# Kernel tuning notes

Hardware: AMD Instinct MI355X
Metric: run time of the kernel (lower is better)

The kernel has to match this reference:

```python
import jax, jax.numpy as jnp
import numpy as np

K = 16

def _pairwise_sqdist(a, b):
    # a:[B,n,3] b:[B,m,3] -> [B,n,m]
    return (jnp.sum(a * a, -1)[:, :, None] + jnp.sum(b * b, -1)[:, None, :]
            - 2.0 * jnp.einsum('bnd,bmd->bnm', a, b))

def _group(x, idx):
    # x:[B,N,C], idx:[B,M,K] -> [B,M,K,C]
    return jax.vmap(lambda xb, ib: xb[ib])(x, idx)

def _gather(x, idx):
    # x:[B,N,C], idx:[B,M] -> [B,M,C]
    return jax.vmap(lambda xb, ib: xb[ib])(x, idx)

def _knn_idx(pos, k):
    p = jax.lax.stop_gradient(pos)
    d = _pairwise_sqdist(p, p)
    return jax.lax.top_k(-d, k)[1]

def _leaky(v):
    return jnp.where(v >= 0, v, 0.2 * v)

def _edge_conv(x, pos, w_self, w_edge, idx=None):
    if idx is None:
        idx = _knn_idx(pos, K)
    nx = _group(x, idx)                      # [B,N,K,C]
    npos = _group(pos, idx)                  # [B,N,K,3]
    rel = pos[:, :, None, :] - npos
    d2 = jnp.sum(rel * rel, -1, keepdims=True)
    h = jnp.concatenate([nx, rel, d2], -1)   # [B,N,K,C+4]
    term_n = jnp.mean(h @ w_edge, axis=2)
    return _leaky(x @ w_self + term_n)

def _fps(pos, npoint):
    # furthest point sampling, starts at index 0 (matches pointnet2 CUDA op)
    pos = jax.lax.stop_gradient(pos)
    B, N, _ = pos.shape
    def body(carry, _):
        dists, far = carry
        c = jnp.take_along_axis(pos, far[:, None, None], axis=1)  # [B,1,3]
        d = jnp.sum((pos - c) ** 2, -1)
        dists = jnp.minimum(dists, d)
        return (dists, jnp.argmax(dists, axis=1).astype(jnp.int32)), far
    init = (jnp.full((B, N), 1e10, pos.dtype), jnp.zeros((B,), jnp.int32))
    _, idxs = jax.lax.scan(body, init, None, length=npoint)
    return jnp.transpose(idxs)  # [B,npoint]

def _three_nn(unknown, known):
    d = _pairwise_sqdist(unknown, known)
    negd, idx = jax.lax.top_k(-d, 3)
    dist = jnp.maximum(-negd, 0.0)  # squared dists, as in pointnet2 kernel
    return jax.lax.stop_gradient(dist), idx  # three_nn is non-differentiable

def _interp_weights(dist):
    recip = 1.0 / (dist + 1e-8)
    return recip / jnp.sum(recip, axis=2, keepdims=True)

def _three_interp(feat, idx, weight):
    g = _group(feat, idx)  # [B,n,3,C]
    return jnp.sum(weight[..., None] * g, axis=2)

def _forward(x, pos, w_self0, w_edge0, w_self1, w_edge1, w_self2, w_edge2,
             w_up1, b_up1, w_upc1_self, w_upc1_edge,
             w_up0, b_up0, w_upc0_self, w_upc0_edge, w_out, b_out):
    feat0 = _edge_conv(x, pos, w_self0, w_edge0)
    pos0 = pos
    n1 = pos0.shape[1] // 2
    idx1 = _fps(pos0, n1)
    pos1 = _gather(pos0, idx1)
    feat1 = _edge_conv(_gather(feat0, idx1), pos1, w_self1, w_edge1)
    n2 = pos1.shape[1] // 2
    idx2 = _fps(pos1, n2)
    pos2 = _gather(pos1, idx2)
    feat2 = _edge_conv(_gather(feat1, idx2), pos2, w_self2, w_edge2)
    dist, idx = _three_nn(pos1, pos2)
    w = _interp_weights(dist)
    cat1 = jnp.concatenate([_three_interp(feat2, idx, w), feat1], -1)
    feat_up1 = _leaky(cat1 @ w_up1 + b_up1)
    feat_up1 = _edge_conv(feat_up1, pos1, w_upc1_self, w_upc1_edge)
    dist, idx = _three_nn(pos0, pos1)
    w = _interp_weights(dist)
    cat0 = jnp.concatenate([_three_interp(feat_up1, idx, w), feat0], -1)
    feat_up0 = _leaky(cat0 @ w_up0 + b_up0)
    feat_out = _edge_conv(feat_up0, pos0, w_upc0_self, w_upc0_edge)
    return feat_out @ w_out + b_out

def setup_inputs() -> dict:
    B, N, CIN, D = 2, 8192, 4, 64
    key = jax.random.key(0)
    ks = jax.random.split(key, 20)
    def w(k, fin, fout):
        return jax.random.normal(k, (fin, fout), jnp.float32) / np.sqrt(fin)
    return {
        'x': jax.random.normal(ks[0], (B, N, CIN), jnp.float32),
        'pos': jax.random.normal(ks[1], (B, N, 3), jnp.float32),
        'w_self0': w(ks[2], CIN, D),        'w_edge0': w(ks[3], CIN + 4, D),
        'w_self1': w(ks[4], D, 2 * D),      'w_edge1': w(ks[5], D + 4, 2 * D),
        'w_self2': w(ks[6], 2 * D, 4 * D),  'w_edge2': w(ks[7], 2 * D + 4, 4 * D),
        'w_up1': w(ks[8], 6 * D, 2 * D),    'b_up1': jnp.zeros((2 * D,), jnp.float32),
        'w_upc1_self': w(ks[9], 2 * D, 2 * D), 'w_upc1_edge': w(ks[10], 2 * D + 4, 2 * D),
        'w_up0': w(ks[11], 3 * D, D),       'b_up0': jnp.zeros((D,), jnp.float32),
        'w_upc0_self': w(ks[12], D, D),     'w_upc0_edge': w(ks[13], D + 4, D),
        'w_out': w(ks[14], D, 128),         'b_out': jnp.zeros((128,), jnp.float32),
    }

def reference(x, pos, w_self0, w_edge0, w_self1, w_edge1, w_self2, w_edge2,
              w_up1, b_up1, w_upc1_self, w_upc1_edge,
              w_up0, b_up0, w_upc0_self, w_upc0_edge, w_out, b_out):
    return _forward(x, pos, w_self0, w_edge0, w_self1, w_edge1, w_self2, w_edge2,
                    w_up1, b_up1, w_upc1_self, w_upc1_edge,
                    w_up0, b_up0, w_upc0_self, w_upc0_edge, w_out, b_out)
```

## Files before the change

### kernel.cpp

```cpp
#include <hip/hip_runtime.h>
#include <cstdint>

typedef unsigned long long u64;

static __device__ __forceinline__ float leakyf(float v) { return v >= 0.f ? v : 0.2f * v; }

__global__ void pack_kernel(const float* __restrict__ pos, int total, float4* __restrict__ out)
{
  int i = blockIdx.x * 256 + threadIdx.x;
  if (i >= total) return;
  float x = pos[i*3+0], y = pos[i*3+1], z = pos[i*3+2];
  out[i] = make_float4(x, y, z, (x*x + y*y) + z*z);
}

template<int CTRL>
static __device__ __forceinline__ u64 dpp_max_u64_step(u64 x)
{
  unsigned lo = (unsigned)x, hi = (unsigned)(x >> 32);
  unsigned ylo = (unsigned)__builtin_amdgcn_update_dpp((int)lo, (int)lo, CTRL, 0xF, 0xF, false);
  unsigned yhi = (unsigned)__builtin_amdgcn_update_dpp((int)hi, (int)hi, CTRL, 0xF, 0xF, false);
  u64 y = ((u64)yhi << 32) | (u64)ylo;
  return x > y ? x : y;
}
static __device__ __forceinline__ u64 wave64_max_u64(u64 x)
{
  x = dpp_max_u64_step<0x111>(x);
  x = dpp_max_u64_step<0x112>(x);
  x = dpp_max_u64_step<0x114>(x);
  x = dpp_max_u64_step<0x118>(x);
  x = dpp_max_u64_step<0x142>(x);
  x = dpp_max_u64_step<0x143>(x);
  unsigned lo = (unsigned)__builtin_amdgcn_readlane((int)(unsigned)x, 63);
  unsigned hi = (unsigned)__builtin_amdgcn_readlane((int)(unsigned)(x >> 32), 63);
  return ((u64)hi << 32) | (u64)lo;
}

template<int N, int NPOINT>
__global__ __launch_bounds__(256) void fps_kernel(const float* __restrict__ pos,
                                                  int* __restrict__ out_idx,
                                                  float* __restrict__ out_pos,
                                                  float4* __restrict__ out_pp)
{
  constexpr int BLOCK = 256;
  constexpr int NPT = N / BLOCK;
  const int b = blockIdx.x;
  const float* P = pos + (size_t)b * N * 3;
  int* oi = out_idx + (size_t)b * NPOINT;
  float* op = out_pos + (size_t)b * NPOINT * 3;
  float4* opp = out_pp + (size_t)b * NPOINT;

  __shared__ float4 spos[N];
  __shared__ __align__(16) u64 redk[2][4];

  const int t = threadIdx.x;
  const int lane = t & 63;
  const int wv = t >> 6;

  float px[NPT], py[NPT], pz[NPT], dist[NPT];
  unsigned iv[NPT];
#pragma unroll
  for (int j = 0; j < NPT; ++j) {
    int i = t + j * BLOCK;
    float x = P[i*3+0], y = P[i*3+1], z = P[i*3+2];
    spos[i] = make_float4(x, y, z, (x*x + y*y) + z*z);
    px[j] = x; py[j] = y; pz[j] = z; dist[j] = 1e10f;
    iv[j] = 0xFFFFFFFFu - (unsigned)i;
  }
  if (t == 0) oi[0] = 0;
  __syncthreads();

  int far = 0;
  for (int it = 1; it < NPOINT; ++it) {
    const float4 c = spos[far];
    if (t == ((it - 1) & (BLOCK - 1))) {
      op[(it-1)*3+0] = c.x; op[(it-1)*3+1] = c.y; op[(it-1)*3+2] = c.z;
      opp[it-1] = c;
    }
    float bd = -1.f; unsigned biv = 0u;
#pragma unroll
    for (int j = 0; j < NPT; ++j) {
      float dx = px[j] - c.x, dy = py[j] - c.y, dz = pz[j] - c.z;
      float d  = fmaf(dz, dz, fmaf(dy, dy, dx * dx));
      float nd = fminf(dist[j], d);
      dist[j] = nd;
      bool bt = nd > bd;
      bd  = bt ? nd : bd;
      biv = bt ? iv[j] : biv;
    }
    u64 key = ((u64)__float_as_uint(bd) << 32) | (u64)biv;
    key = wave64_max_u64(key);
    const int par = it & 1;
    if (lane == 0) redk[par][wv] = key;
    __syncthreads();
    const ulonglong2 p01 = *reinterpret_cast<const ulonglong2*>(&redk[par][0]);
    const ulonglong2 p23 = *reinterpret_cast<const ulonglong2*>(&redk[par][2]);
    u64 k0 = p01.x > p01.y ? p01.x : p01.y;
    u64 k1 = p23.x > p23.y ? p23.x : p23.y;
    key = k0 > k1 ? k0 : k1;
    far = (int)(0xFFFFFFFFu - (unsigned)(key & 0xFFFFFFFFull));
    if (t == 0) oi[it] = far;
  }
  {
    const float4 c = spos[far];
    if (t == ((NPOINT - 1) & (BLOCK - 1))) {
      op[(NPOINT-1)*3+0] = c.x; op[(NPOINT-1)*3+1] = c.y; op[(NPOINT-1)*3+2] = c.z;
      opp[NPOINT-1] = c;
    }
  }
}

template<int G>
__global__ __launch_bounds__(256) void knn_kernel(const float4* __restrict__ pp, int M,
                                                  int* __restrict__ out)
{
  const int b = blockIdx.y;
  const float4* P = pp + (size_t)b * M;
  const int tid = threadIdx.x;
  constexpr int QPB = 256 / G;
  const int q = blockIdx.x * QPB + tid / G;
  const int seg = tid % G;

  __shared__ float4 tile[512];

  const float4 qp = P[q];
  const float qx = qp.x, qy = qp.y, qz = qp.z, qq = qp.w;

  float a[16]; int id[16];
#pragma unroll
  for (int j = 0; j < 16; ++j) { a[j] = 3.4e38f; id[j] = 0x7fffffff; }

  for (int t0 = 0; t0 < M; t0 += 512) {
    __syncthreads();
    tile[tid]       = P[t0 + tid];
    tile[tid + 256] = P[t0 + tid + 256];
    __syncthreads();
#pragma unroll 4
    for (int i = seg; i < 512; i += G) {
      float4 c = tile[i];
      float d = (qq + c.w) - 2.f * ((qx*c.x + qy*c.y) + qz*c.z);
      int gi = t0 + i;
      if (d < a[15]) {
        bool cc[16];
#pragma unroll
        for (int j = 0; j < 16; ++j) cc[j] = d < a[j];
#pragma unroll
        for (int j = 15; j >= 1; --j) {
          a[j]  = cc[j-1] ? a[j-1]  : (cc[j] ? d  : a[j]);
          id[j] = cc[j-1] ? id[j-1] : (cc[j] ? gi : id[j]);
        }
        if (cc[0]) { a[0] = d; id[0] = gi; }
      }
    }
  }
#pragma unroll
  for (int s = G/2; s >= 1; s >>= 1) {
    float bd[16]; int bi[16];
#pragma unroll
    for (int j = 0; j < 16; ++j) { bd[j] = __shfl_xor(a[j], s); bi[j] = __shfl_xor(id[j], s); }
#pragma unroll
    for (int j = 0; j < 16; ++j) {
      float od = bd[15-j]; int ob = bi[15-j];
      bool take = (od < a[j]) || (od == a[j] && ob < id[j]);
      a[j]  = take ? od : a[j];
      id[j] = take ? ob : id[j];
    }
#pragma unroll
    for (int st = 8; st >= 1; st >>= 1) {
#pragma unroll
      for (int j = 0; j < 16; ++j) {
        if ((j & st) == 0) {
          const int j2 = j + st;
          bool sw = (a[j2] < a[j]) || (a[j2] == a[j] && id[j2] < id[j]);
          float lod = sw ? a[j2] : a[j];  int loi = sw ? id[j2] : id[j];
          float hid = sw ? a[j]  : a[j2]; int hii = sw ? id[j]  : id[j2];
          a[j] = lod; id[j] = loi; a[j2] = hid; id[j2] = hii;
        }
      }
    }
  }
  if (seg == 0) {
    int* opp = out + ((size_t)b * M + q) * 16;
#pragma unroll
    for (int j = 0; j < 16; ++j) opp[j] = id[j];
  }
}

template<int G>
__global__ __launch_bounds__(256) void three_nn_kernel(const float4* __restrict__ qpp,
                                                       const float4* __restrict__ kpp,
                                                       int Mq, int Mk,
                                                       int* __restrict__ oidx, float* __restrict__ ow)
{
  const int b = blockIdx.y;
  const float4* Q  = qpp + (size_t)b * Mq;
  const float4* Kp = kpp + (size_t)b * Mk;
  const int tid = threadIdx.x;
  constexpr int QPB = 256 / G;
  const int q = blockIdx.x * QPB + tid / G;
  const int seg = tid % G;

  __shared__ float4 tile[512];

  const float4 qp = Q[q];
  const float qx = qp.x, qy = qp.y, qz = qp.z, qq = qp.w;

  float a[4]; int id[4];
#pragma unroll
  for (int j = 0; j < 4; ++j) { a[j] = 3.4e38f; id[j] = 0x7fffffff; }

  for (int t0 = 0; t0 < Mk; t0 += 512) {
    __syncthreads();
    tile[tid]       = Kp[t0 + tid];
    tile[tid + 256] = Kp[t0 + tid + 256];
    __syncthreads();
#pragma unroll 4
    for (int i = seg; i < 512; i += G) {
      float4 c = tile[i];
      float d = (qq + c.w) - 2.f * ((qx*c.x + qy*c.y) + qz*c.z);
      int gi = t0 + i;
      if (d < a[3]) {
        bool c0 = d < a[0], c1 = d < a[1], c2 = d < a[2];
        a[3]  = c2 ? a[2]  : d;                id[3] = c2 ? id[2] : gi;
        a[2]  = c1 ? a[1]  : (c2 ? d  : a[2]); id[2] = c1 ? id[1] : (c2 ? gi : id[2]);
        a[1]  = c0 ? a[0]  : (c1 ? d  : a[1]); id[1] = c0 ? id[0] : (c1 ? gi : id[1]);
        if (c0) { a[0] = d; id[0] = gi; }
      }
    }
  }
#pragma unroll
  for (int s = G/2; s >= 1; s >>= 1) {
    float bd[4]; int bi[4];
#pragma unroll
    for (int j = 0; j < 4; ++j) { bd[j] = __shfl_xor(a[j], s); bi[j] = __shfl_xor(id[j], s); }
#pragma unroll
    for (int j = 0; j < 4; ++j) {
      float od = bd[3-j]; int ob = bi[3-j];
      bool take = (od < a[j]) || (od == a[j] && ob < id[j]);
      a[j]  = take ? od : a[j];
      id[j] = take ? ob : id[j];
    }
#pragma unroll
    for (int st = 2; st >= 1; st >>= 1) {
#pragma unroll
      for (int j = 0; j < 4; ++j) {
        if ((j & st) == 0) {
          const int j2 = j + st;
          bool sw = (a[j2] < a[j]) || (a[j2] == a[j] && id[j2] < id[j]);
          float lod = sw ? a[j2] : a[j];  int loi = sw ? id[j2] : id[j];
          float hid = sw ? a[j]  : a[j2]; int hii = sw ? id[j]  : id[j2];
          a[j] = lod; id[j] = loi; a[j2] = hid; id[j2] = hii;
        }
      }
    }
  }
  if (seg == 0) {
    float d0 = fmaxf(a[0], 0.f), d1 = fmaxf(a[1], 0.f), d2 = fmaxf(a[2], 0.f);
    float r0 = 1.f/(d0 + 1e-8f), r1 = 1.f/(d1 + 1e-8f), r2 = 1.f/(d2 + 1e-8f);
    float s = (r0 + r1) + r2;
    size_t o = ((size_t)b * Mq + q) * 3;
    oidx[o+0] = id[0]; oidx[o+1] = id[1]; oidx[o+2] = id[2];
    ow[o+0] = r0/s; ow[o+1] = r1/s; ow[o+2] = r2/s;
  }
}

__global__ void hbar_kernel(const float* __restrict__ x, const float* __restrict__ pos,
                            const int* __restrict__ idx, int Mlvl, int C, int B,
                            float* __restrict__ out)
{
  const int Ct = C + 4;
  const int tot = B * Mlvl * Ct;
  int e = blockIdx.x * 256 + threadIdx.x;
  if (e >= tot) return;
  const int c  = e % Ct;
  const int p  = e / Ct;
  const int b  = p / Mlvl;
  const int lm = p % Mlvl;
  const int* ip = idx + (size_t)p * 16;
  float s = 0.f;
  if (c < C) {
    const float* xb = x + (size_t)b * Mlvl * C;
#pragma unroll 4
    for (int k = 0; k < 16; ++k) s += xb[(size_t)ip[k] * C + c];
  } else if (c < C + 3) {
    const int dd = c - C;
    const float* pb = pos + (size_t)b * Mlvl * 3;
    const float pc = pb[lm*3 + dd];
#pragma unroll 4
    for (int k = 0; k < 16; ++k) s += pc - pb[ip[k]*3 + dd];
  } else {
    const float* pb = pos + (size_t)b * Mlvl * 3;
    const float px = pb[lm*3+0], py = pb[lm*3+1], pz = pb[lm*3+2];
#pragma unroll 4
    for (int k = 0; k < 16; ++k) {
      int n = ip[k];
      float dx = px - pb[n*3+0], dy = py - pb[n*3+1], dz = pz - pb[n*3+2];
      s += (dx*dx + dy*dy) + dz*dz;
    }
  }
  out[e] = s * 0.0625f;
}

__global__ void interp_kernel(const float* __restrict__ f, const int* __restrict__ nidx,
                              const float* __restrict__ nw, int Mq, int Msub, int C, int B,
                              float* __restrict__ out)
{
  const int tot = B * Mq * C;
  int e = blockIdx.x * 256 + threadIdx.x;
  if (e >= tot) return;
  const int c = e % C;
  const int p = e / C;
  const int b = p / Mq;
  const float* fb = f + (size_t)b * Msub * C;
  const int* ip   = nidx + (size_t)p * 3;
  const float* wp = nw   + (size_t)p * 3;
  out[e] = (wp[0] * fb[(size_t)ip[0]*C + c] + wp[1] * fb[(size_t)ip[1]*C + c])
         +  wp[2] * fb[(size_t)ip[2]*C + c];
}

__global__ void gather_kernel(const float* __restrict__ src, const int* __restrict__ idx,
                              int Mq, int Msrc, int C, int B, float* __restrict__ dst)
{
  const int tot = B * Mq * C;
  int e = blockIdx.x * 256 + threadIdx.x;
  if (e >= tot) return;
  const int c = e % C;
  const int p = e / C;
  const int b = p / Mq;
  dst[e] = src[((size_t)b * Msrc + idx[p]) * C + c];
}

__global__ __launch_bounds__(256) void gemm_kernel(const float* __restrict__ A, int Ka,
                                                   const float* __restrict__ B2, int Kb,
                                                   const float* __restrict__ W1,
                                                   const float* __restrict__ W2,
                                                   const float* __restrict__ bias,
                                                   float* __restrict__ out,
                                                   int M, int F, int act)
{
  __shared__ __align__(16) float As[16][64];
  __shared__ __align__(16) float Ws[16][64];
  const int tid  = threadIdx.x;
  const int row0 = blockIdx.x * 64;
  const int col0 = blockIdx.y * 64;
  const int tx = tid & 15, ty = tid >> 4;
  const int K = Ka + Kb;
  float acc[4][4] = {};
  for (int k0 = 0; k0 < K; k0 += 16) {
#pragma unroll
    for (int i = 0; i < 4; ++i) {
      int e = tid + i * 256;
      int m = e & 63, kk = e >> 6;
      int k = k0 + kk;
      float v = 0.f;
      if (k < Ka)     v = A [(size_t)(row0 + m) * Ka + k];
      else if (k < K) v = B2[(size_t)(row0 + m) * Kb + (k - Ka)];
      As[kk][m] = v;
      float wv = 0.f;
      if (k < Ka)     wv = W1[(size_t)k * F + col0 + m];
      else if (k < K) wv = W2[(size_t)(k - Ka) * F + col0 + m];
      Ws[kk][m] = wv;
    }
    __syncthreads();
#pragma unroll
    for (int kk = 0; kk < 16; ++kk) {
      const float4 a4 = *reinterpret_cast<const float4*>(&As[kk][ty * 4]);
      const float4 b4 = *reinterpret_cast<const float4*>(&Ws[kk][tx * 4]);
      const float av[4] = {a4.x, a4.y, a4.z, a4.w};
      const float bv[4] = {b4.x, b4.y, b4.z, b4.w};
#pragma unroll
      for (int i2 = 0; i2 < 4; ++i2)
#pragma unroll
        for (int j2 = 0; j2 < 4; ++j2)
          acc[i2][j2] = fmaf(av[i2], bv[j2], acc[i2][j2]);
    }
    __syncthreads();
  }
#pragma unroll
  for (int i2 = 0; i2 < 4; ++i2) {
    int r = row0 + ty * 4 + i2;
#pragma unroll
    for (int j2 = 0; j2 < 4; ++j2) {
      int cc = col0 + tx * 4 + j2;
      float v = acc[i2][j2];
      if (bias) v += bias[cc];
      if (act)  v = leakyf(v);
      out[(size_t)r * F + cc] = v;
    }
  }
}

extern "C" void kernel_launch(void* const* d_in, const int* in_sizes, int n_in,
                              void* d_out, int out_size, void* d_ws, size_t ws_size,
                              hipStream_t stream)
{
  (void)in_sizes; (void)n_in; (void)out_size; (void)ws_size;
  const float* x          = (const float*)d_in[0];
  const float* pos        = (const float*)d_in[1];
  const float* w_self0    = (const float*)d_in[2];
  const float* w_edge0    = (const float*)d_in[3];
  const float* w_self1    = (const float*)d_in[4];
  const float* w_edge1    = (const float*)d_in[5];
  const float* w_self2    = (const float*)d_in[6];
  const float* w_edge2    = (const float*)d_in[7];
  const float* w_up1      = (const float*)d_in[8];
  const float* b_up1      = (const float*)d_in[9];
  const float* w_upc1s    = (const float*)d_in[10];
  const float* w_upc1e    = (const float*)d_in[11];
  const float* w_up0      = (const float*)d_in[12];
  const float* b_up0      = (const float*)d_in[13];
  const float* w_upc0s    = (const float*)d_in[14];
  const float* w_upc0e    = (const float*)d_in[15];
  const float* w_out      = (const float*)d_in[16];
  const float* b_out      = (const float*)d_in[17];
  float* out = (float*)d_out;

  char* ws = (char*)d_ws;
  size_t off = 0;
  auto alloc = [&](size_t nbytes) -> void* {
    off = (off + 255) & ~(size_t)255;
    void* p = ws + off;
    off += nbytes;
    return p;
  };
  int*    knn0   = (int*)   alloc((size_t)2*8192*16*4);
  int*    knn1   = (int*)   alloc((size_t)2*4096*16*4);
  int*    knn2   = (int*)   alloc((size_t)2*2048*16*4);
  int*    idx1   = (int*)   alloc((size_t)2*4096*4);
  int*    idx2   = (int*)   alloc((size_t)2*2048*4);
  float*  pos1   = (float*) alloc((size_t)2*4096*3*4);
  float*  pos2   = (float*) alloc((size_t)2*2048*3*4);
  float4* pp0    = (float4*)alloc((size_t)2*8192*16);
  float4* pp1    = (float4*)alloc((size_t)2*4096*16);
  float4* pp2    = (float4*)alloc((size_t)2*2048*16);
  float*  feat0  = (float*) alloc((size_t)2*8192*64*4);
  float*  feat0g = (float*) alloc((size_t)2*4096*64*4);
  float*  feat1  = (float*) alloc((size_t)2*4096*128*4);
  float*  feat1g = (float*) alloc((size_t)2*2048*128*4);
  float*  feat2  = (float*) alloc((size_t)2*2048*256*4);
  int*    nn1i   = (int*)   alloc((size_t)2*4096*3*4);
  float*  nn1w   = (float*) alloc((size_t)2*4096*3*4);
  int*    nn0i   = (int*)   alloc((size_t)2*8192*3*4);
  float*  nn0w   = (float*) alloc((size_t)2*8192*3*4);
  float*  interp = (float*) alloc((size_t)2*4096*256*4);
  float*  hbar   = (float*) alloc((size_t)2*8192*68*4);
  float*  fupa   = (float*) alloc((size_t)2*4096*128*4);
  float*  fup1   = (float*) alloc((size_t)2*4096*128*4);
  float*  fout   = (float*) alloc((size_t)2*8192*64*4);

  pack_kernel<<<64, 256, 0, stream>>>(pos, 2*8192, pp0);
  knn_kernel<16><<<dim3(512, 2), 256, 0, stream>>>(pp0, 8192, knn0);
  hbar_kernel<<<512, 256, 0, stream>>>(x, pos, knn0, 8192, 4, 2, hbar);
  gemm_kernel<<<dim3(256, 1), 256, 0, stream>>>(x, 4, hbar, 8, w_self0, w_edge0, nullptr,
                                                feat0, 16384, 64, 1);
  fps_kernel<8192, 4096><<<2, 256, 0, stream>>>(pos, idx1, pos1, pp1);
  gather_kernel<<<2048, 256, 0, stream>>>(feat0, idx1, 4096, 8192, 64, 2, feat0g);
  knn_kernel<16><<<dim3(256, 2), 256, 0, stream>>>(pp1, 4096, knn1);
  hbar_kernel<<<2176, 256, 0, stream>>>(feat0g, pos1, knn1, 4096, 64, 2, hbar);
  gemm_kernel<<<dim3(128, 2), 256, 0, stream>>>(feat0g, 64, hbar, 68, w_self1, w_edge1, nullptr,
                                                feat1, 8192, 128, 1);
  fps_kernel<4096, 2048><<<2, 256, 0, stream>>>(pos1, idx2, pos2, pp2);
  gather_kernel<<<2048, 256, 0, stream>>>(feat1, idx2, 2048, 4096, 128, 2, feat1g);
  knn_kernel<16><<<dim3(128, 2), 256, 0, stream>>>(pp2, 2048, knn2);
  hbar_kernel<<<2112, 256, 0, stream>>>(feat1g, pos2, knn2, 2048, 128, 2, hbar);
  gemm_kernel<<<dim3(64, 4), 256, 0, stream>>>(feat1g, 128, hbar, 132, w_self2, w_edge2, nullptr,
                                               feat2, 4096, 256, 1);
  three_nn_kernel<16><<<dim3(256, 2), 256, 0, stream>>>(pp1, pp2, 4096, 2048, nn1i, nn1w);
  interp_kernel<<<8192, 256, 0, stream>>>(feat2, nn1i, nn1w, 4096, 2048, 256, 2, interp);
  gemm_kernel<<<dim3(128, 2), 256, 0, stream>>>(interp, 256, feat1, 128,
                                                w_up1, w_up1 + (size_t)256 * 128, b_up1,
                                                fupa, 8192, 128, 1);
  hbar_kernel<<<4224, 256, 0, stream>>>(fupa, pos1, knn1, 4096, 128, 2, hbar);
  gemm_kernel<<<dim3(128, 2), 256, 0, stream>>>(fupa, 128, hbar, 132, w_upc1s, w_upc1e, nullptr,
                                                fup1, 8192, 128, 1);
  three_nn_kernel<16><<<dim3(512, 2), 256, 0, stream>>>(pp0, pp1, 8192, 4096, nn0i, nn0w);
  interp_kernel<<<8192, 256, 0, stream>>>(fup1, nn0i, nn0w, 8192, 4096, 128, 2, interp);
  gemm_kernel<<<dim3(256, 1), 256, 0, stream>>>(interp, 128, feat0, 64,
                                                w_up0, w_up0 + (size_t)128 * 64, b_up0,
                                                fupa, 16384, 64, 1);
  hbar_kernel<<<4352, 256, 0, stream>>>(fupa, pos, knn0, 8192, 64, 2, hbar);
  gemm_kernel<<<dim3(256, 1), 256, 0, stream>>>(fupa, 64, hbar, 68, w_upc0s, w_upc0e, nullptr,
                                                fout, 16384, 64, 1);
  gemm_kernel<<<dim3(256, 2), 256, 0, stream>>>(fout, 64, nullptr, 0, w_out, nullptr, b_out,
                                                out, 16384, 128, 0);
}
```

Before: 5.958 ms.

## Fuse FPS with independent kNN/hbar/three-NN work into shared launches

Measured after the change: 5.650 ms. 1.05x faster.

```diff
diff --git a/kernel.cpp b/kernel.cpp
--- a/kernel.cpp
+++ b/kernel.cpp
@@ -4,14 +4,6 @@
 typedef unsigned long long u64;
 
 static __device__ __forceinline__ float leakyf(float v) { return v >= 0.f ? v : 0.2f * v; }
-
-__global__ void pack_kernel(const float* __restrict__ pos, int total, float4* __restrict__ out)
-{
-  int i = blockIdx.x * 256 + threadIdx.x;
-  if (i >= total) return;
-  float x = pos[i*3+0], y = pos[i*3+1], z = pos[i*3+2];
-  out[i] = make_float4(x, y, z, (x*x + y*y) + z*z);
-}
 
 template<int CTRL>
 static __device__ __forceinline__ u64 dpp_max_u64_step(u64 x)
@@ -36,35 +28,29 @@
 }
 
 template<int N, int NPOINT>
-__global__ __launch_bounds__(256) void fps_kernel(const float* __restrict__ pos,
-                                                  int* __restrict__ out_idx,
-                                                  float* __restrict__ out_pos,
-                                                  float4* __restrict__ out_pp)
+static __device__ void fps_body(const float* __restrict__ P,
+                                int* __restrict__ oi, float* __restrict__ op,
+                                float4* __restrict__ opp,
+                                float4* spos, u64* redk )
 {
   constexpr int BLOCK = 256;
   constexpr int NPT = N / BLOCK;
-  const int b = blockIdx.x;
-  const float* P = pos + (size_t)b * N * 3;
-  int* oi = out_idx + (size_t)b * NPOINT;
-  float* op = out_pos + (size_t)b * NPOINT * 3;
-  float4* opp = out_pp + (size_t)b * NPOINT;
-
-  __shared__ float4 spos[N];
-  __shared__ __align__(16) u64 redk[2][4];
-
   const int t = threadIdx.x;
   const int lane = t & 63;
   const int wv = t >> 6;
 
+  for (int k = 0; k < NPT; ++k) {
+    int i = t * NPT + k;
+    float x = P[i*3+0], y = P[i*3+1], z = P[i*3+2];
+    spos[i] = make_float4(x, y, z, (x*x + y*y) + z*z);
+  }
   float px[NPT], py[NPT], pz[NPT], dist[NPT];
-  unsigned iv[NPT];
 #pragma unroll
   for (int j = 0; j < NPT; ++j) {
     int i = t + j * BLOCK;
     float x = P[i*3+0], y = P[i*3+1], z = P[i*3+2];
-    spos[i] = make_float4(x, y, z, (x*x + y*y) + z*z);
     px[j] = x; py[j] = y; pz[j] = z; dist[j] = 1e10f;
-    iv[j] = 0xFFFFFFFFu - (unsigned)i;
+    asm volatile("" : "+v"(px[j]), "+v"(py[j]), "+v"(pz[j]));
   }
   if (t == 0) oi[0] = 0;
   __syncthreads();
@@ -85,15 +71,15 @@
       dist[j] = nd;
       bool bt = nd > bd;
       bd  = bt ? nd : bd;
-      biv = bt ? iv[j] : biv;
+      biv = bt ? (0xFFFFFFFFu - (unsigned)(t + j * BLOCK)) : biv;
     }
     u64 key = ((u64)__float_as_uint(bd) << 32) | (u64)biv;
     key = wave64_max_u64(key);
     const int par = it & 1;
-    if (lane == 0) redk[par][wv] = key;
-    __syncthreads();
-    const ulonglong2 p01 = *reinterpret_cast<const ulonglong2*>(&redk[par][0]);
-    const ulonglong2 p23 = *reinterpret_cast<const ulonglong2*>(&redk[par][2]);
+    if (lane == 0) redk[par*4 + wv] = key;
+    __syncthreads();
+    const ulonglong2 p01 = *reinterpret_cast<const ulonglong2*>(&redk[par*4 + 0]);
+    const ulonglong2 p23 = *reinterpret_cast<const ulonglong2*>(&redk[par*4 + 2]);
     u64 k0 = p01.x > p01.y ? p01.x : p01.y;
     u64 k1 = p23.x > p23.y ? p23.x : p23.y;
     key = k0 > k1 ? k0 : k1;
@@ -110,20 +96,17 @@
 }
 
 template<int G>
-__global__ __launch_bounds__(256) void knn_kernel(const float4* __restrict__ pp, int M,
-                                                  int* __restrict__ out)
-{
-  const int b = blockIdx.y;
-  const float4* P = pp + (size_t)b * M;
+static __device__ void knn_body(const float* __restrict__ pos, int M,
+                                int* __restrict__ out, float4* tile, int xb, int b)
+{
+  const float* P = pos + (size_t)b * M * 3;
   const int tid = threadIdx.x;
   constexpr int QPB = 256 / G;
-  const int q = blockIdx.x * QPB + tid / G;
+  const int q = xb * QPB + tid / G;
   const int seg = tid % G;
 
-  __shared__ float4 tile[512];
-
-  const float4 qp = P[q];
-  const float qx = qp.x, qy = qp.y, qz = qp.z, qq = qp.w;
+  const float qx = P[q*3+0], qy = P[q*3+1], qz = P[q*3+2];
+  const float qq = (qx*qx + qy*qy) + qz*qz;
 
   float a[16]; int id[16];
 #pragma unroll
@@ -131,8 +114,11 @@
 
   for (int t0 = 0; t0 < M; t0 += 512) {
     __syncthreads();
-    tile[tid]       = P[t0 + tid];
-    tile[tid + 256] = P[t0 + tid + 256];
+    for (int i = tid; i < 512; i += 256) {
+      int gi = t0 + i;
+      float x = P[gi*3+0], y = P[gi*3+1], z = P[gi*3+2];
+      tile[i] = make_float4(x, y, z, (x*x + y*y) + z*z);
+    }
     __syncthreads();
 #pragma unroll 4
     for (int i = seg; i < 512; i += G) {
@@ -185,21 +171,26 @@
   }
 }
 
+__global__ __launch_bounds__(256) void knn_kernel(const float* __restrict__ pos, int M,
+                                                  int* __restrict__ out)
+{
+  __shared__ float4 tile[512];
+  knn_body<16>(pos, M, out, tile, blockIdx.x, blockIdx.y);
+}
+
 template<int G>
-__global__ __launch_bounds__(256) void three_nn_kernel(const float4* __restrict__ qpp,
-                                                       const float4* __restrict__ kpp,
-                                                       int Mq, int Mk,
-                                                       int* __restrict__ oidx, float* __restrict__ ow)
-{
-  const int b = blockIdx.y;
+static __device__ void three_nn_body(const float4* __restrict__ qpp,
+                                     const float4* __restrict__ kpp,
+                                     int Mq, int Mk,
+                                     int* __restrict__ oidx, float* __restrict__ ow,
+                                     float4* tile, int xb, int b)
+{
   const float4* Q  = qpp + (size_t)b * Mq;
   const float4* Kp = kpp + (size_t)b * Mk;
   const int tid = threadIdx.x;
   constexpr int QPB = 256 / G;
-  const int q = blockIdx.x * QPB + tid / G;
+  const int q = xb * QPB + tid / G;
   const int seg = tid % G;
-
-  __shared__ float4 tile[512];
 
   const float4 qp = Q[q];
   const float qx = qp.x, qy = qp.y, qz = qp.z, qq = qp.w;
@@ -263,13 +254,21 @@
   }
 }
 
-__global__ void hbar_kernel(const float* __restrict__ x, const float* __restrict__ pos,
-                            const int* __restrict__ idx, int Mlvl, int C, int B,
-                            float* __restrict__ out)
+__global__ __launch_bounds__(256) void three_nn_kernel(const float4* __restrict__ qpp,
+                                                       const float4* __restrict__ kpp,
+                                                       int Mq, int Mk,
+                                                       int* __restrict__ oidx, float* __restrict__ ow)
+{
+  __shared__ float4 tile[512];
+  three_nn_body<16>(qpp, kpp, Mq, Mk, oidx, ow, tile, blockIdx.x, blockIdx.y);
+}
+
+static __device__ void hbar_body(const float* __restrict__ x, const float* __restrict__ pos,
+                                 const int* __restrict__ idx, int Mlvl, int C, int B,
+                                 float* __restrict__ out, int e)
 {
   const int Ct = C + 4;
   const int tot = B * Mlvl * Ct;
-  int e = blockIdx.x * 256 + threadIdx.x;
   if (e >= tot) return;
   const int c  = e % Ct;
   const int p  = e / Ct;
@@ -298,6 +297,65 @@
     }
   }
   out[e] = s * 0.0625f;
+}
+
+__global__ void hbar_kernel(const float* __restrict__ x, const float* __restrict__ pos,
+                            const int* __restrict__ idx, int Mlvl, int C, int B,
+                            float* __restrict__ out)
+{
+  hbar_body(x, pos, idx, Mlvl, C, B, out, blockIdx.x * 256 + threadIdx.x);
+}
+
+__global__ __launch_bounds__(256, 1) void fused1_kernel(const float* __restrict__ pos,
+    int* __restrict__ idx1, float* __restrict__ pos1, float4* __restrict__ pp1,
+    float4* __restrict__ pp0, int* __restrict__ knn0)
+{
+  __shared__ __align__(16) char sm[8192 * 16 + 64];
+  const int blk = blockIdx.x;
+  if (blk < 2) {
+    fps_body<8192, 4096>(pos + (size_t)blk * 8192 * 3,
+                         idx1 + (size_t)blk * 4096,
+                         pos1 + (size_t)blk * 4096 * 3,
+                         pp1 + (size_t)blk * 4096,
+                         (float4*)sm, (u64*)(sm + 8192 * 16));
+  } else if (blk < 1026) {
+    const int i = blk - 2;
+    knn_body<16>(pos, 8192, knn0, (float4*)sm, i & 511, i >> 9);
+  } else {
+    const int i = (blk - 1026) * 256 + threadIdx.x;
+    if (i < 2 * 8192) {
+      float x = pos[i*3+0], y = pos[i*3+1], z = pos[i*3+2];
+      pp0[i] = make_float4(x, y, z, (x*x + y*y) + z*z);
+    }
+  }
+}
+
+__global__ __launch_bounds__(256, 1) void fused2_kernel(const float* __restrict__ pos,
+    const float* __restrict__ pos1, const float* __restrict__ x,
+    const int* __restrict__ knn0, float* __restrict__ hbar,
+    int* __restrict__ idx2, float* __restrict__ pos2, float4* __restrict__ pp2,
+    int* __restrict__ knn1,
+    const float4* __restrict__ pp0, const float4* __restrict__ pp1,
+    int* __restrict__ nn0i, float* __restrict__ nn0w)
+{
+  __shared__ __align__(16) char sm[4096 * 16 + 64];
+  const int blk = blockIdx.x;
+  if (blk < 2) {
+    fps_body<4096, 2048>(pos1 + (size_t)blk * 4096 * 3,
+                         idx2 + (size_t)blk * 2048,
+                         pos2 + (size_t)blk * 2048 * 3,
+                         pp2 + (size_t)blk * 2048,
+                         (float4*)sm, (u64*)(sm + 4096 * 16));
+  } else if (blk < 514) {
+    const int i = blk - 2;
+    knn_body<16>(pos1, 4096, knn1, (float4*)sm, i & 255, i >> 8);
+  } else if (blk < 1026) {
+    const int e = (blk - 514) * 256 + threadIdx.x;
+    hbar_body(x, pos, knn0, 8192, 4, 2, hbar, e);
+  } else {
+    const int i = blk - 1026;
+    three_nn_body<16>(pp0, pp1, 8192, 4096, nn0i, nn0w, (float4*)sm, i & 511, i >> 9);
+  }
 }
 
 __global__ void interp_kernel(const float* __restrict__ f, const int* __restrict__ nidx,
@@ -447,24 +505,21 @@
   float*  fup1   = (float*) alloc((size_t)2*4096*128*4);
   float*  fout   = (float*) alloc((size_t)2*8192*64*4);
 
-  pack_kernel<<<64, 256, 0, stream>>>(pos, 2*8192, pp0);
-  knn_kernel<16><<<dim3(512, 2), 256, 0, stream>>>(pp0, 8192, knn0);
-  hbar_kernel<<<512, 256, 0, stream>>>(x, pos, knn0, 8192, 4, 2, hbar);
+  fused1_kernel<<<1090, 256, 0, stream>>>(pos, idx1, pos1, pp1, pp0, knn0);
+  fused2_kernel<<<2050, 256, 0, stream>>>(pos, pos1, x, knn0, hbar,
+                                          idx2, pos2, pp2, knn1, pp0, pp1, nn0i, nn0w);
   gemm_kernel<<<dim3(256, 1), 256, 0, stream>>>(x, 4, hbar, 8, w_self0, w_edge0, nullptr,
                                                 feat0, 16384, 64, 1);
-  fps_kernel<8192, 4096><<<2, 256, 0, stream>>>(pos, idx1, pos1, pp1);
   gather_kernel<<<2048, 256, 0, stream>>>(feat0, idx1, 4096, 8192, 64, 2, feat0g);
-  knn_kernel<16><<<dim3(256, 2), 256, 0, stream>>>(pp1, 4096, knn1);
   hbar_kernel<<<2176, 256, 0, stream>>>(feat0g, pos1, knn1, 4096, 64, 2, hbar);
   gemm_kernel<<<dim3(128, 2), 256, 0, stream>>>(feat0g, 64, hbar, 68, w_self1, w_edge1, nullptr,
                                                 feat1, 8192, 128, 1);
-  fps_kernel<4096, 2048><<<2, 256, 0, stream>>>(pos1, idx2, pos2, pp2);
   gather_kernel<<<2048, 256, 0, stream>>>(feat1, idx2, 2048, 4096, 128, 2, feat1g);
-  knn_kernel<16><<<dim3(128, 2), 256, 0, stream>>>(pp2, 2048, knn2);
+  knn_kernel<<<dim3(128, 2), 256, 0, stream>>>(pos2, 2048, knn2);
   hbar_kernel<<<2112, 256, 0, stream>>>(feat1g, pos2, knn2, 2048, 128, 2, hbar);
   gemm_kernel<<<dim3(64, 4), 256, 0, stream>>>(feat1g, 128, hbar, 132, w_self2, w_edge2, nullptr,
                                                feat2, 4096, 256, 1);
-  three_nn_kernel<16><<<dim3(256, 2), 256, 0, stream>>>(pp1, pp2, 4096, 2048, nn1i, nn1w);
+  three_nn_kernel<<<dim3(256, 2), 256, 0, stream>>>(pp1, pp2, 4096, 2048, nn1i, nn1w);
   interp_kernel<<<8192, 256, 0, stream>>>(feat2, nn1i, nn1w, 4096, 2048, 256, 2, interp);
   gemm_kernel<<<dim3(128, 2), 256, 0, stream>>>(interp, 256, feat1, 128,
                                                 w_up1, w_up1 + (size_t)256 * 128, b_up1,
@@ -472,7 +527,6 @@
   hbar_kernel<<<4224, 256, 0, stream>>>(fupa, pos1, knn1, 4096, 128, 2, hbar);
   gemm_kernel<<<dim3(128, 2), 256, 0, stream>>>(fupa, 128, hbar, 132, w_upc1s, w_upc1e, nullptr,
                                                 fup1, 8192, 128, 1);
-  three_nn_kernel<16><<<dim3(512, 2), 256, 0, stream>>>(pp0, pp1, 8192, 4096, nn0i, nn0w);
   interp_kernel<<<8192, 256, 0, stream>>>(fup1, nn0i, nn0w, 8192, 4096, 128, 2, interp);
   gemm_kernel<<<dim3(256, 1), 256, 0, stream>>>(interp, 128, feat0, 64,
                                                 w_up0, w_up0 + (size_t)128 * 64, b_up0,
```
